# Performance work log

Measured on AMD Instinct MI355X. Metric: run time of the kernel, lower is better.

Reference implementation:

```python
import jax, jax.numpy as jnp
import numpy as np

SIZE = 7  # grid size; H = W = SIZE


def setup_inputs() -> dict:
    key = jax.random.key(0)
    k1, k2, k3, k4 = jax.random.split(key, 4)
    N, C = 256, 2048
    x = jax.random.normal(k1, (N, C, SIZE, SIZE), dtype=jnp.float32)
    mask = jax.random.uniform(k2, (N, SIZE, SIZE), dtype=jnp.float32)
    W = jax.random.normal(k3, (2, 2 * C), dtype=jnp.float32) * 0.02
    b = jax.random.normal(k4, (2,), dtype=jnp.float32) * 0.02
    return {"x": x, "mask": mask, "W": W, "b": b}


def reference(x, mask, W, b):
    N, C, H, Wd = x.shape
    HW = H * Wd
    size = float(H)
    # (N, HW, C) tokens
    reduced_x = jnp.transpose(x.reshape(N, C, HW), (0, 2, 1))
    m = mask.reshape(N, HW)
    thr = jnp.mean(m, axis=1, keepdims=True)  # curr_coef = 1.0
    binary_mask = (m > thr).astype(x.dtype)  # (N, HW)
    # mean over channels of masked tokens, then argmax over positions
    masked_mean = jnp.mean(reduced_x * binary_mask[:, :, None], axis=-1)  # (N, HW)
    max_index = jnp.argmax(masked_mean, axis=-1)  # (N,)
    batch_idx = jnp.arange(N)
    max_features = reduced_x[batch_idx, max_index]  # (N, C)
    # concat(max_feature, token) -> tiny linear 2C -> 2 with ReLU
    disc = jnp.concatenate(
        [jnp.broadcast_to(max_features[:, None, :], (N, HW, C)), reduced_x], axis=-1
    )  # (N, HW, 2C)
    preds_coord = jax.nn.relu(jnp.einsum('npc,oc->npo', disc, W) + b)  # (N, HW, 2)
    # zero out prediction at the anchor position
    preds_coord = preds_coord.at[batch_idx, max_index].set(0.0)
    # polar-coordinate targets relative to anchor
    ii, jj = jnp.meshgrid(jnp.arange(H), jnp.arange(Wd), indexing='ij')
    label = jnp.stack([ii, jj], axis=-1).astype(x.dtype).reshape(HW, 2)  # (HW, 2)
    basic_anchor = label[max_index][:, None, :]  # (N, 1, 2)
    rel = (label[None, :, :] - basic_anchor) / size  # (N, HW, 2)
    relative_dist = jnp.sqrt(jnp.sum(rel ** 2, axis=-1))  # (N, HW)
    relative_angle = jnp.arctan2(rel[:, :, 1], rel[:, :, 0])
    relative_angle = (relative_angle / jnp.float32(np.pi) + 1.0) / 2.0  # (N, HW)
    preds_dist = preds_coord[:, :, 0]
    preds_angle = preds_coord[:, :, 1]
    dist_loss = (preds_dist - relative_dist) ** 2
    gap = preds_angle - relative_angle
    gap = jnp.where(gap < 0, gap + 1.0, gap)
    gap = gap - jnp.mean(gap, axis=-1, keepdims=True)
    angle_loss = gap ** 2
    return (dist_loss + angle_loss).reshape(N, H, Wd)
```

## Files before the change

kernel.cpp:

```cpp
#include <hip/hip_runtime.h>
#include <math.h>

#define N_     256
#define C_     2048
#define HW_    49
#define CHUNKS 8
#define CPB    (C_/CHUNKS)
#define TILE_C 64
#define NG     5

__global__ __launch_bounds__(256) void k_reduce(const float* __restrict__ x,
                                                const float* __restrict__ Wm,
                                                float* __restrict__ part) {
  const int chunk = blockIdx.x;
  const int n     = blockIdx.y;
  const int t     = threadIdx.x;

  __shared__ float4 tile4[(TILE_C*HW_)/4];
  __shared__ float  wt[NG][TILE_C];
  float* tile = (float*)tile4;

  const int g = t / HW_;
  const int p = t - g*HW_;

  float acc = 0.f;

  for (int tc = 0; tc < CPB; tc += TILE_C) {
    const int c0 = chunk*CPB + tc;
    const float4* src = (const float4*)(x + ((size_t)n*C_ + (size_t)c0)*HW_);
    #pragma unroll
    for (int i = 0; i < 4; ++i) {
      int idx = t + i*256;
      if (idx < (TILE_C*HW_)/4) tile4[idx] = src[idx];
    }
    for (int i = t; i < NG*TILE_C; i += 256) {
      int gg = i / TILE_C, cc = i - gg*TILE_C;
      float w;
      if (gg == 0) w = 1.f;
      else {
        int row  = (gg-1) & 1;
        int half = (gg-1) >> 1;
        w = Wm[row*(2*C_) + half*C_ + c0 + cc];
      }
      wt[gg][cc] = w;
    }
    __syncthreads();
    if (g < NG) {
      #pragma unroll 8
      for (int c = 0; c < TILE_C; ++c)
        acc = fmaf(tile[c*HW_ + p], wt[g][c], acc);
    }
    __syncthreads();
  }
  if (g < NG)
    part[((size_t)n*CHUNKS + chunk)*(NG*HW_) + t] = acc;
}

__global__ __launch_bounds__(256) void k_final(const float* __restrict__ part,
                                               const float* __restrict__ mask,
                                               const float* __restrict__ b,
                                               float* __restrict__ out) {
  const int n = blockIdx.x;
  const int t = threadIdx.x;
  __shared__ float red[NG*HW_];

  if (t < NG*HW_) {
    float a = 0.f;
    #pragma unroll
    for (int ch = 0; ch < CHUNKS; ++ch)
      a += part[((size_t)n*CHUNKS + ch)*(NG*HW_) + t];
    red[t] = a;
  }
  __syncthreads();

  if (t < 64) {
    const int  p   = t;
    const bool act = (p < HW_);

    float m = act ? mask[n*HW_ + p] : 0.f;
    float tot = m;
    #pragma unroll
    for (int off = 32; off; off >>= 1) tot += __shfl_xor(tot, off);
    const float thr = tot / 49.f;

    float s  = act ? red[0*HW_ + p] : 0.f;
    float mm = act ? ((m > thr) ? (s * (1.f/2048.f)) : 0.f) : -INFINITY;
    float best = mm;
    int   bidx = act ? p : 64;
    #pragma unroll
    for (int off = 32; off; off >>= 1) {
      float ov = __shfl_xor(best, off);
      int   oi = __shfl_xor(bidx, off);
      if (ov > best || (ov == best && oi < bidx)) { best = ov; bidx = oi; }
    }
    const int mi = bidx;

    const float u0mi = red[1*HW_ + mi];
    const float u1mi = red[2*HW_ + mi];

    float pred0 = 0.f, pred1 = 0.f;
    if (act) {
      pred0 = fmaxf(u0mi + red[3*HW_ + p] + b[0], 0.f);
      pred1 = fmaxf(u1mi + red[4*HW_ + p] + b[1], 0.f);
      if (p == mi) { pred0 = 0.f; pred1 = 0.f; }
    }

    const int ii = p / 7,  jj = p - ii*7;
    const int ai = mi / 7, aj = mi - ai*7;
    const float ri = (float)(ii - ai) / 7.f;
    const float rj = (float)(jj - aj) / 7.f;
    const float dist = sqrtf(ri*ri + rj*rj);
    const float ang  = (atan2f(rj, ri) / 3.14159274101257324f + 1.f) * 0.5f;

    float gap = pred1 - ang;
    if (gap < 0.f) gap += 1.f;
    float gsum = act ? gap : 0.f;
    #pragma unroll
    for (int off = 32; off; off >>= 1) gsum += __shfl_xor(gsum, off);
    const float gmean = gsum / 49.f;

    if (act) {
      const float dl = pred0 - dist;
      const float ga = gap - gmean;
      out[n*HW_ + p] = dl*dl + ga*ga;
    }
  }
}

extern "C" void kernel_launch(void* const* d_in, const int* in_sizes, int n_in,
                              void* d_out, int out_size, void* d_ws, size_t ws_size,
                              hipStream_t stream) {
  const float* x    = (const float*)d_in[0];
  const float* mask = (const float*)d_in[1];
  const float* Wm   = (const float*)d_in[2];
  const float* b    = (const float*)d_in[3];
  float* out  = (float*)d_out;
  float* part = (float*)d_ws;

  dim3 g1(CHUNKS, N_);
  k_reduce<<<g1, 256, 0, stream>>>(x, Wm, part);
  k_final<<<N_, 256, 0, stream>>>(part, mask, b, out);
}
```

Baseline: 162.6 us.

## Double-buffer x tiles via async global_load_lds and compute five sums per thread

Replaces the synchronous register-staged tile copy with direct global-to-LDS async loads into a double buffer, so the next tile is fetched while the current one is reduced. Weights are preloaded once per block as float4, and a single wave computes all five dot products per position instead of spreading them across five thread groups. Chunk count drops from 8 to 4, giving each block more tiles to pipeline over. The trade-off is that only one wave of 256 threads does the arithmetic, with fewer blocks in the grid, and correctness rests on hand-written waitcnt and barrier ordering.

```diff
diff --git a/kernel.cpp b/kernel.cpp
--- a/kernel.cpp
+++ b/kernel.cpp
@@ -4,10 +4,31 @@
 #define N_     256
 #define C_     2048
 #define HW_    49
-#define CHUNKS 8
+#define CHUNKS 4
 #define CPB    (C_/CHUNKS)
 #define TILE_C 64
+#define NTILE  (CPB/TILE_C)
 #define NG     5
+#define TILE_BYTES (TILE_C*HW_*4)
+
+__device__ __forceinline__ void cp16(const void* gptr, unsigned lds_off) {
+  __builtin_amdgcn_global_load_lds(
+      (const __attribute__((address_space(1))) unsigned int*)gptr,
+      (__attribute__((address_space(3))) unsigned int*)lds_off,
+      16, 0, 0);
+}
+
+__device__ __forceinline__ void stage_tile(const float* src, unsigned lb,
+                                           int wave, int lane) {
+  const char* s = (const char*)src;
+  #pragma unroll
+  for (int i = 0; i < 3; ++i) {
+    const int seg = wave + i*4;
+    cp16(s + seg*1024 + lane*16, lb + (unsigned)(seg*1024));
+  }
+  if (lane < 4)
+    cp16(s + 12288 + wave*64 + lane*16, lb + (unsigned)(12288 + wave*64));
+}
 
 __global__ __launch_bounds__(256) void k_reduce(const float* __restrict__ x,
                                                 const float* __restrict__ Wm,
@@ -15,45 +36,73 @@
   const int chunk = blockIdx.x;
   const int n     = blockIdx.y;
   const int t     = threadIdx.x;
+  const int wave  = t >> 6;
+  const int lane  = t & 63;
 
-  __shared__ float4 tile4[(TILE_C*HW_)/4];
-  __shared__ float  wt[NG][TILE_C];
-  float* tile = (float*)tile4;
+  __shared__ __align__(16) float  buf[2][TILE_C*HW_];
+  __shared__ float4 wt4[CPB];
 
-  const int g = t / HW_;
-  const int p = t - g*HW_;
+  const unsigned lb0 = (unsigned)(size_t)&buf[0][0];
+  const unsigned lb1 = (unsigned)(size_t)&buf[1][0];
 
-  float acc = 0.f;
+  const float* xbase = x + ((size_t)n*C_ + (size_t)chunk*CPB)*HW_;
 
-  for (int tc = 0; tc < CPB; tc += TILE_C) {
-    const int c0 = chunk*CPB + tc;
-    const float4* src = (const float4*)(x + ((size_t)n*C_ + (size_t)c0)*HW_);
-    #pragma unroll
-    for (int i = 0; i < 4; ++i) {
-      int idx = t + i*256;
-      if (idx < (TILE_C*HW_)/4) tile4[idx] = src[idx];
+  for (int c = t; c < CPB; c += 256) {
+    const int gc = chunk*CPB + c;
+    float4 w;
+    w.x = Wm[0*(2*C_)       + gc];
+    w.y = Wm[1*(2*C_)       + gc];
+    w.z = Wm[0*(2*C_) + C_  + gc];
+    w.w = Wm[1*(2*C_) + C_  + gc];
+    wt4[c] = w;
+  }
+
+  stage_tile(xbase, lb0, wave, lane);
+
+  asm volatile("s_waitcnt lgkmcnt(0)" ::: "memory");
+  __builtin_amdgcn_s_barrier();
+
+  const int  p   = lane;
+  const bool act = (wave == 0) && (lane < HW_);
+
+  float a0 = 0.f, a1 = 0.f, a2 = 0.f, a3 = 0.f, a4 = 0.f;
+
+  for (int tt = 0; tt < NTILE; ++tt) {
+    if (tt < NTILE-1) {
+      stage_tile(xbase + (size_t)(tt+1)*TILE_C*HW_,
+                 (tt & 1) ? lb0 : lb1, wave, lane);
+      asm volatile("s_waitcnt vmcnt(4)" ::: "memory");
+    } else {
+      asm volatile("s_waitcnt vmcnt(0)" ::: "memory");
     }
-    for (int i = t; i < NG*TILE_C; i += 256) {
-      int gg = i / TILE_C, cc = i - gg*TILE_C;
-      float w;
-      if (gg == 0) w = 1.f;
-      else {
-        int row  = (gg-1) & 1;
-        int half = (gg-1) >> 1;
-        w = Wm[row*(2*C_) + half*C_ + c0 + cc];
+    __builtin_amdgcn_s_barrier();
+
+    if (act) {
+      const float*  tl = buf[tt & 1];
+      const float4* wp = &wt4[tt*TILE_C];
+      #pragma unroll 16
+      for (int c = 0; c < TILE_C; ++c) {
+        const float  v = tl[c*HW_ + p];
+        const float4 w = wp[c];
+        a0 += v;
+        a1 = fmaf(v, w.x, a1);
+        a2 = fmaf(v, w.y, a2);
+        a3 = fmaf(v, w.z, a3);
+        a4 = fmaf(v, w.w, a4);
       }
-      wt[gg][cc] = w;
     }
-    __syncthreads();
-    if (g < NG) {
-      #pragma unroll 8
-      for (int c = 0; c < TILE_C; ++c)
-        acc = fmaf(tile[c*HW_ + p], wt[g][c], acc);
-    }
-    __syncthreads();
+    asm volatile("s_waitcnt lgkmcnt(0)" ::: "memory");
+    __builtin_amdgcn_s_barrier();
   }
-  if (g < NG)
-    part[((size_t)n*CHUNKS + chunk)*(NG*HW_) + t] = acc;
+
+  if (act) {
+    float* dst = part + ((size_t)n*CHUNKS + chunk)*(NG*HW_);
+    dst[0*HW_ + p] = a0;
+    dst[1*HW_ + p] = a1;
+    dst[2*HW_ + p] = a2;
+    dst[3*HW_ + p] = a3;
+    dst[4*HW_ + p] = a4;
+  }
 }
 
 __global__ __launch_bounds__(256) void k_final(const float* __restrict__ part,
```

New measurement: 159.2 us. 2.1% less time.
